# Kernel optimization log

Measured on AMD Instinct MI355X. Metric: run time of the kernel, lower is better.

## Reference

```python
import jax, jax.numpy as jnp
import numpy as np

B, N, DIM, H, HD, MLP = 32, 257, 1024, 16, 64, 4096
SCALE = HD ** -0.5


def _ln(x, w, b, eps=1e-5):
    m = x.mean(-1, keepdims=True)
    v = ((x - m) ** 2).mean(-1, keepdims=True)
    return (x - m) * jax.lax.rsqrt(v + eps) * w + b


def _quick_gelu(x):
    return x * jax.nn.sigmoid(1.702 * x)


def setup_inputs() -> dict:
    key = jax.random.key(0)
    ks = jax.random.split(key, 8)
    p = lambda k, s: jax.random.normal(k, s, jnp.float32) * 0.02
    return {
        'hidden_states': jax.random.normal(ks[0], (B, N, DIM), jnp.float32),
        'ln1_w': jnp.ones((DIM,), jnp.float32), 'ln1_b': jnp.zeros((DIM,), jnp.float32),
        'Wq': p(ks[1], (DIM, DIM)), 'bq': jnp.zeros((DIM,), jnp.float32),
        'Wk': p(ks[2], (DIM, DIM)), 'bk': jnp.zeros((DIM,), jnp.float32),
        'Wv': p(ks[3], (DIM, DIM)), 'bv': jnp.zeros((DIM,), jnp.float32),
        'Wo': p(ks[4], (DIM, DIM)), 'bo': jnp.zeros((DIM,), jnp.float32),
        'ln2_w': jnp.ones((DIM,), jnp.float32), 'ln2_b': jnp.zeros((DIM,), jnp.float32),
        'fc1_w': p(ks[5], (MLP, DIM)), 'fc1_b': jnp.zeros((MLP,), jnp.float32),
        'fc2_w': p(ks[6], (DIM, MLP)), 'fc2_b': jnp.zeros((DIM,), jnp.float32),
    }


def reference(hidden_states, ln1_w, ln1_b, Wq, bq, Wk, bk, Wv, bv, Wo, bo,
              ln2_w, ln2_b, fc1_w, fc1_b, fc2_w, fc2_b):
    x = _ln(hidden_states, ln1_w, ln1_b)            # [B,N,DIM]
    def heads(y):                                    # [B,N,DIM] -> [B,H,N,HD]
        return y.reshape(B, N, H, HD).transpose(0, 2, 1, 3)
    q = heads((x @ Wq.T + bq) * SCALE)
    k = heads(x @ Wk.T + bk)
    v = heads(x @ Wv.T + bv)
    attn_weights = jax.nn.softmax(jnp.einsum('bhnd,bhmd->bhnm', q, k), axis=-1)  # [B,H,N,N]
    ctx = jnp.einsum('bhnm,bhmd->bhnd', attn_weights, v)
    pre_proj = ctx.transpose(0, 2, 1, 3).reshape(B, N, DIM)
    attn_output = pre_proj @ Wo.T + bo
    h = hidden_states + attn_output
    residual = h
    h = _ln(h, ln2_w, ln2_b)
    h = _quick_gelu(h @ fc1_w.T + fc1_b) @ fc2_w.T + fc2_b
    hidden_out = residual + h
    # reuse_start='before_mlp': returns (pre_proj, cache_states=None, hidden, attn_weights, qkvs=None, reuse_map=None)
    return pre_proj, hidden_out, attn_weights
```

## Files before the change

kernel.cpp:

```cpp
#include <hip/hip_runtime.h>

typedef unsigned short u16;
typedef __bf16 bf16x8 __attribute__((ext_vector_type(8)));
typedef float f32x4 __attribute__((ext_vector_type(4)));
typedef unsigned short u16x8 __attribute__((ext_vector_type(8)));
typedef unsigned short u16x4 __attribute__((ext_vector_type(4)));

#define NBATCH 32
#define NTOK   257
#define DMODEL 1024
#define NHEAD  16
#define HDIM   64
#define DMLP   4096
#define MTOK   (NBATCH*NTOK)
#define MPAD   8320

__device__ __forceinline__ u16 f2bf(float f){
    unsigned int u = __float_as_uint(f);
    u = u + 0x7fffu + ((u >> 16) & 1u);
    return (u16)(u >> 16);
}

__device__ __forceinline__ f32x4 mfma16(bf16x8 a, bf16x8 b, f32x4 c){
    return __builtin_amdgcn_mfma_f32_16x16x32_bf16(a, b, c, 0, 0, 0);
}

__device__ __forceinline__ void gload16(const void* g, void* l){
    __builtin_amdgcn_global_load_lds(
        (const __attribute__((address_space(1))) unsigned int*)g,
        (__attribute__((address_space(3))) unsigned int*)l, 16, 0, 0);
}

__device__ __forceinline__ float waveSum64(float v){
    #pragma unroll
    for (int d = 1; d < 64; d <<= 1) v += __shfl_xor(v, d);
    return v;
}

__device__ __forceinline__ void xcd_swz(int &bx, int &by){
    int gx = gridDim.x;
    int nwg = gx * gridDim.y;
    int bid = blockIdx.y * gx + blockIdx.x;
    int wg = (bid & 7) * (nwg >> 3) + (bid >> 3);
    bx = wg % gx; by = wg / gx;
}

__global__ __launch_bounds__(256) void cvt_all(
        const float* __restrict__ wq, const float* __restrict__ wk,
        const float* __restrict__ wv, const float* __restrict__ wo,
        const float* __restrict__ f1, const float* __restrict__ f2,
        u16* __restrict__ dst){
    int b = blockIdx.x;
    const float* s; int rb; float sc = 1.0f;
    if (b < 1024)      { s = wq; rb = 0;    sc = 0.125f; }
    else if (b < 2048) { s = wk; rb = 1024; }
    else if (b < 3072) { s = wv; rb = 2048; }
    else if (b < 4096) { s = wo; rb = 3072; }
    else if (b < 8192) { s = f1; rb = 4096; }
    else               { s = f2; rb = 8192; }
    size_t li = ((size_t)(b - rb)*256 + threadIdx.x)*4;
    float4 v = *(const float4*)(s + li);
    u16x4 o = { f2bf(v.x*sc), f2bf(v.y*sc), f2bf(v.z*sc), f2bf(v.w*sc) };
    *(u16x4*)(dst + (size_t)b*1024 + threadIdx.x*4) = o;
}

__global__ __launch_bounds__(256) void build_bqkv(
        const float* __restrict__ bq, const float* __restrict__ bk,
        const float* __restrict__ bv, float* __restrict__ o){
    int i = blockIdx.x*256 + threadIdx.x;
    float v = (i < 1024) ? bq[i]*0.125f : ((i < 2048) ? bk[i-1024] : bv[i-2048]);
    o[i] = v;
}

__global__ __launch_bounds__(256) void ln_kernel(const float* __restrict__ x,
                                                 const float* __restrict__ w,
                                                 const float* __restrict__ b,
                                                 u16* __restrict__ y){
    int row = blockIdx.x, tid = threadIdx.x;
    float4 v = ((const float4*)(x + (size_t)row*DMODEL))[tid];
    float s = v.x + v.y + v.z + v.w;
    s = waveSum64(s);
    __shared__ float red[8];
    int wv = tid >> 6;
    if ((tid & 63) == 0) red[wv] = s;
    __syncthreads();
    float mean = (red[0]+red[1]+red[2]+red[3]) * (1.0f/1024.0f);
    float dx = v.x-mean, dy = v.y-mean, dz = v.z-mean, dw = v.w-mean;
    float s2 = dx*dx + dy*dy + dz*dz + dw*dw;
    s2 = waveSum64(s2);
    if ((tid & 63) == 0) red[4+wv] = s2;
    __syncthreads();
    float var = (red[4]+red[5]+red[6]+red[7]) * (1.0f/1024.0f);
    float rs = rsqrtf(var + 1e-5f);
    float4 wl = ((const float4*)w)[tid];
    float4 bl = ((const float4*)b)[tid];
    u16x4 o = { f2bf(dx*rs*wl.x + bl.x), f2bf(dy*rs*wl.y + bl.y),
                f2bf(dz*rs*wl.z + bl.z), f2bf(dw*rs*wl.w + bl.w) };
    ((u16x4*)(y + (size_t)row*DMODEL))[tid] = o;
}

template<int EPI>
__global__ __launch_bounds__(256) void gemm_bt(
        const u16* __restrict__ A, const u16* __restrict__ Wt,
        const float* __restrict__ bias, u16* __restrict__ outb,
        int K, int Nn, int Mvalid){
    __shared__ __align__(16) u16 As[128*64];
    __shared__ __align__(16) u16 Bs[128*64];
    int tid = threadIdx.x, lane = tid & 63, w = tid >> 6;
    int wr = w >> 1, wc = w & 1;
    int bx, by; xcd_swz(bx, by);
    int m0 = by*128, n0 = bx*128;
    int lrow = lane & 15, lk = lane >> 4;
    const f32x4 fz = {0.f,0.f,0.f,0.f};
    f32x4 acc[4][4];
    #pragma unroll
    for (int i = 0; i < 4; i++)
        #pragma unroll
        for (int j = 0; j < 4; j++) acc[i][j] = fz;

    const size_t Ks = (size_t)K;
    int so = w*1024 + lane*16;
    for (int kt = 0; kt < K; kt += 64){
        #pragma unroll
        for (int i = 0; i < 4; i++){
            int o = i*4096 + so;
            int row = o >> 7;
            int gsl = ((o >> 4) & 7) ^ (row & 7);
            gload16(A  + (size_t)(m0+row)*Ks + kt + gsl*8, &As[i*2048 + w*512]);
            gload16(Wt + (size_t)(n0+row)*Ks + kt + gsl*8, &Bs[i*2048 + w*512]);
        }
        __syncthreads();
        #pragma unroll
        for (int kk = 0; kk < 2; kk++){
            bf16x8 af[4], bfr[4];
            #pragma unroll
            for (int mi = 0; mi < 4; mi++){
                int row = wr*64 + mi*16 + lrow;
                int sl = (kk*4 + lk) ^ (row & 7);
                af[mi] = *(const bf16x8*)&As[row*64 + sl*8];
            }
            #pragma unroll
            for (int ni = 0; ni < 4; ni++){
                int row = wc*64 + ni*16 + lrow;
                int sl = (kk*4 + lk) ^ (row & 7);
                bfr[ni] = *(const bf16x8*)&Bs[row*64 + sl*8];
            }
            #pragma unroll
            for (int mi = 0; mi < 4; mi++)
                #pragma unroll
                for (int ni = 0; ni < 4; ni++)
                    acc[mi][ni] = mfma16(af[mi], bfr[ni], acc[mi][ni]);
        }
        __syncthreads();
    }
    #pragma unroll
    for (int mi = 0; mi < 4; mi++){
        #pragma unroll
        for (int ni = 0; ni < 4; ni++){
            int col = n0 + wc*64 + ni*16 + lrow;
            float bi = bias[col];
            #pragma unroll
            for (int r = 0; r < 4; r++){
                int row = m0 + wr*64 + mi*16 + lk*4 + r;
                if (row < Mvalid){
                    float v = acc[mi][ni][r] + bi;
                    size_t idx = (size_t)row*Nn + col;
                    if (EPI == 0){
                        outb[idx] = f2bf(v);
                    } else {
                        float g = v / (1.f + __expf(-1.702f*v));
                        outb[idx] = f2bf(g);
                    }
                }
            }
        }
    }
}

__global__ __launch_bounds__(256) void gemm_n64(
        const u16* __restrict__ A, const u16* __restrict__ Wt,
        const float* __restrict__ bias, const float* __restrict__ addsrc,
        float* __restrict__ outf,
        int K, int Nn, int Mvalid){
    __shared__ __align__(16) u16 As[128*64];
    __shared__ __align__(16) u16 Bs[64*64];
    int tid = threadIdx.x, lane = tid & 63, w = tid >> 6;
    int wr = w >> 1, wc = w & 1;
    int bx, by; xcd_swz(bx, by);
    int m0 = by*128, n0 = bx*64;
    int lrow = lane & 15, lk = lane >> 4;
    const f32x4 fz = {0.f,0.f,0.f,0.f};
    f32x4 acc[4][2];
    #pragma unroll
    for (int i = 0; i < 4; i++){ acc[i][0] = fz; acc[i][1] = fz; }

    const size_t Ks = (size_t)K;
    int so = w*1024 + lane*16;
    for (int kt = 0; kt < K; kt += 64){
        #pragma unroll
        for (int i = 0; i < 4; i++){
            int o = i*4096 + so;
            int row = o >> 7;
            int gsl = ((o >> 4) & 7) ^ (row & 7);
            gload16(A + (size_t)(m0+row)*Ks + kt + gsl*8, &As[i*2048 + w*512]);
        }
        #pragma unroll
        for (int i = 0; i < 2; i++){
            int o = i*4096 + so;
            int row = o >> 7;
            int gsl = ((o >> 4) & 7) ^ (row & 7);
            gload16(Wt + (size_t)(n0+row)*Ks + kt + gsl*8, &Bs[i*2048 + w*512]);
        }
        __syncthreads();
        #pragma unroll
        for (int kk = 0; kk < 2; kk++){
            bf16x8 af[4], bfr[2];
            #pragma unroll
            for (int mi = 0; mi < 4; mi++){
                int row = wr*64 + mi*16 + lrow;
                int sl = (kk*4 + lk) ^ (row & 7);
                af[mi] = *(const bf16x8*)&As[row*64 + sl*8];
            }
            #pragma unroll
            for (int ni = 0; ni < 2; ni++){
                int row = wc*32 + ni*16 + lrow;
                int sl = (kk*4 + lk) ^ (row & 7);
                bfr[ni] = *(const bf16x8*)&Bs[row*64 + sl*8];
            }
            #pragma unroll
            for (int mi = 0; mi < 4; mi++)
                #pragma unroll
                for (int ni = 0; ni < 2; ni++)
                    acc[mi][ni] = mfma16(af[mi], bfr[ni], acc[mi][ni]);
        }
        __syncthreads();
    }
    #pragma unroll
    for (int mi = 0; mi < 4; mi++){
        #pragma unroll
        for (int ni = 0; ni < 2; ni++){
            int col = n0 + wc*32 + ni*16 + lrow;
            float bi = bias[col];
            #pragma unroll
            for (int r = 0; r < 4; r++){
                int row = m0 + wr*64 + mi*16 + lk*4 + r;
                if (row < Mvalid){
                    float v = acc[mi][ni][r] + bi;
                    size_t idx = (size_t)row*Nn + col;
                    outf[idx] = addsrc[idx] + v;
                }
            }
        }
    }
}

__global__ __launch_bounds__(256) void attn_kernel(
        const u16* __restrict__ qkv, float* __restrict__ preproj,
        u16* __restrict__ ctxb, float* __restrict__ attnw){
    __shared__ __align__(16) u16 shm[18432 + 64*296];
    u16* Klds = shm;
    u16* Plds = shm;
    u16* Vt   = shm + 18432;
    int tid = threadIdx.x, lane = tid & 63, w = tid >> 6;
    int bh = blockIdx.x, bq = bh >> 4, hh = bh & 15;
    int q0 = blockIdx.y*64;
    int lrow = lane & 15, lk = lane >> 4;

    size_t base3 = ((size_t)bq*NTOK)*3072 + hh*HDIM;
    for (int c = tid; c < 2176; c += 256){
        int row = c >> 3, slot = c & 7;
        u16x8 kv = {0,0,0,0,0,0,0,0}, vv = {0,0,0,0,0,0,0,0};
        if (row < NTOK){
            kv = *(const u16x8*)(qkv + base3 + 1024 + (size_t)row*3072 + slot*8);
            vv = *(const u16x8*)(qkv + base3 + 2048 + (size_t)row*3072 + slot*8);
        }
        *(u16x8*)&Klds[row*64 + (slot ^ (row & 7))*8] = kv;
        int vr = (row < 256) ? (row ^ (slot << 3)) : row;
        #pragma unroll
        for (int j = 0; j < 8; j++) Vt[(slot*8 + j)*296 + vr] = vv[j];
    }
    for (int i = tid; i < 1536; i += 256){
        int d = i/24, c2 = 272 + (i - d*24);
        Vt[d*296 + c2] = 0;
    }
    int tok = bq*NTOK + q0 + w*16 + lrow;
    const u16* qp = qkv + (size_t)tok*3072 + hh*HDIM;
    bf16x8 qf0 = *(const bf16x8*)(qp + lk*8);
    bf16x8 qf1 = *(const bf16x8*)(qp + 32 + lk*8);
    __syncthreads();

    f32x4 S[17];
    __builtin_amdgcn_s_setprio(1);
    #pragma unroll
    for (int j = 0; j < 17; j++){
        int kcol = j*16 + lrow;
        f32x4 a = {0.f,0.f,0.f,0.f};
        bf16x8 b0 = *(const bf16x8*)&Klds[kcol*64 + ((0 + lk) ^ (kcol & 7))*8];
        a = mfma16(qf0, b0, a);
        bf16x8 b1 = *(const bf16x8*)&Klds[kcol*64 + ((4 + lk) ^ (kcol & 7))*8];
        S[j] = mfma16(qf1, b1, a);
    }
    __builtin_amdgcn_s_setprio(0);
    #pragma unroll
    for (int r = 0; r < 4; r++){
        float mx = -1e30f;
        #pragma unroll
        for (int j = 0; j < 17; j++){
            bool valid = (j < 16) || (lrow == 0);
            mx = fmaxf(mx, valid ? S[j][r] : -1e30f);
        }
        #pragma unroll
        for (int d = 1; d < 16; d <<= 1) mx = fmaxf(mx, __shfl_xor(mx, d));
        float sum = 0.f;
        #pragma unroll
        for (int j = 0; j < 17; j++){
            bool valid = (j < 16) || (lrow == 0);
            float p = valid ? __expf(S[j][r] - mx) : 0.f;
            S[j][r] = p; sum += p;
        }
        #pragma unroll
        for (int d = 1; d < 16; d <<= 1) sum += __shfl_xor(sum, d);
        float inv = 1.f / sum;
        #pragma unroll
        for (int j = 0; j < 17; j++) S[j][r] *= inv;
    }
    __syncthreads();

    for (int idx = tid; idx < 1024; idx += 256){
        int prow = idx >> 4, kk = idx & 15;
        int koff = 16 + kk;
        int slot = ((koff >> 3) ^ (prow >> 2)) & 3;
        Plds[8*2048 + prow*32 + slot*8 + (koff & 7)] = 0;
    }
    #pragma unroll
    for (int r = 0; r < 4; r++){
        int rw = lk*4 + r;
        int qrow = q0 + w*16 + rw;
        bool rowok = qrow < NTOK;
        size_t obase = ((size_t)bh*NTOK + qrow)*NTOK;
        int prow = w*16 + rw;
        #pragma unroll
        for (int j = 0; j < 17; j++){
            int col = j*16 + lrow;
            float p = S[j][r];
            if (rowok && col < NTOK) attnw[obase + col] = p;
            int kstep = col >> 5, koff = col & 31;
            int slot = ((koff >> 3) ^ (prow >> 2)) & 3;
            Plds[kstep*2048 + prow*32 + slot*8 + (koff & 7)] = f2bf(p);
        }
    }
    __syncthreads();

    f32x4 C4[4];
    #pragma unroll
    for (int n = 0; n < 4; n++) C4[n] = (f32x4){0.f,0.f,0.f,0.f};
    __builtin_amdgcn_s_setprio(1);
    #pragma unroll
    for (int ks = 0; ks < 9; ks++){
        int prow = w*16 + lrow;
        int slotp = (lk ^ (lrow >> 2)) & 3;
        bf16x8 pf = *(const bf16x8*)&Plds[ks*2048 + prow*32 + slotp*8];
        #pragma unroll
        for (int n = 0; n < 4; n++){
            int d = n*16 + lrow;
            int xv = (d >> 3) & 7;
            int kbase = ks*32 + lk*8;
            int kl = (ks < 8) ? (kbase ^ (xv << 3)) : kbase;
            bf16x8 vf = *(const bf16x8*)&Vt[d*296 + kl];
            C4[n] = mfma16(pf, vf, C4[n]);
        }
    }
    __builtin_amdgcn_s_setprio(0);
    #pragma unroll
    for (int n = 0; n < 4; n++){
        #pragma unroll
        for (int r = 0; r < 4; r++){
            int qrow = q0 + w*16 + lk*4 + r;
            if (qrow < NTOK){
                int tok2 = bq*NTOK + qrow;
                int d = hh*HDIM + n*16 + lrow;
                float v = C4[n][r];
                preproj[(size_t)tok2*DMODEL + d] = v;
                ctxb[(size_t)tok2*DMODEL + d] = f2bf(v);
            }
        }
    }
}

extern "C" void kernel_launch(void* const* d_in, const int* in_sizes, int n_in,
                              void* d_out, int out_size, void* d_ws, size_t ws_size,
                              hipStream_t stream){
    const float* hidden = (const float*)d_in[0];
    const float* ln1w = (const float*)d_in[1];
    const float* ln1b = (const float*)d_in[2];
    const float* Wq   = (const float*)d_in[3];
    const float* bq   = (const float*)d_in[4];
    const float* Wk   = (const float*)d_in[5];
    const float* bk   = (const float*)d_in[6];
    const float* Wv   = (const float*)d_in[7];
    const float* bv   = (const float*)d_in[8];
    const float* Wo   = (const float*)d_in[9];
    const float* bo   = (const float*)d_in[10];
    const float* ln2w = (const float*)d_in[11];
    const float* ln2b = (const float*)d_in[12];
    const float* fc1w = (const float*)d_in[13];
    const float* fc1b = (const float*)d_in[14];
    const float* fc2w = (const float*)d_in[15];
    const float* fc2b = (const float*)d_in[16];

    float* out0 = (float*)d_out;
    float* out1 = out0 + (size_t)MTOK*DMODEL;
    float* out2 = out1 + (size_t)MTOK*DMODEL;

    char* ws = (char*)d_ws;
    u16* qkvb = (u16*)ws;
    u16* fc1o = (u16*)ws;
    size_t off = (size_t)MPAD*DMLP*2;
    u16* xln  = (u16*)(ws + off);
    u16* ctxb = xln;
    off += (size_t)MPAD*DMODEL*2;
    u16* wbase = (u16*)(ws + off);
    u16* wqkv = wbase;
    u16* wob  = wbase + 3*1048576;
    u16* wf1  = wbase + 4*1048576;
    u16* wf2  = wbase + 8*1048576;
    off += (size_t)12*1048576*2;
    float* bqkv = (float*)(ws + off);

    cvt_all<<<12288, 256, 0, stream>>>(Wq, Wk, Wv, Wo, fc1w, fc2w, wbase);
    build_bqkv<<<12, 256, 0, stream>>>(bq, bk, bv, bqkv);

    ln_kernel<<<MTOK, 256, 0, stream>>>(hidden, ln1w, ln1b, xln);

    gemm_bt<0><<<dim3(24,65), 256, 0, stream>>>(xln, wqkv, bqkv, qkvb, 1024, 3072, MTOK);

    attn_kernel<<<dim3(512,5), 256, 0, stream>>>(qkvb, out0, ctxb, out2);

    gemm_n64<<<dim3(16,65), 256, 0, stream>>>(ctxb, wob, bo, hidden, out1, 1024, 1024, MTOK);

    ln_kernel<<<MTOK, 256, 0, stream>>>(out1, ln2w, ln2b, xln);

    gemm_bt<2><<<dim3(32,65), 256, 0, stream>>>(xln, wf1, fc1b, fc1o, 1024, 4096, MTOK);

    gemm_n64<<<dim3(16,65), 256, 0, stream>>>(fc1o, wf2, fc2b, out1, out1, 4096, 1024, MTOK);
}
```

Baseline: 470.2 us.

## Replace 128x128 GEMM with 256x256 tile, 4-stage LDS pipelined kernel for QKV and FC1

Swaps the single-buffered 128x128 bf16 GEMM used for the QKV and FC1 projections for a 512-thread, 256x256-tile kernel. The new kernel keeps a 4-slot LDS ring with K-steps of 32, issues loads three stages ahead, waits with explicit vmcnt, and raises wave priority around the MFMA block. It also uses a new XCD-aware block remap and pads M to 8448 so it divides into 256-row tiles. The goal is more reuse per loaded tile and overlap of global loads with compute, at the cost of far more LDS and registers, lower occupancy and more wasted padded rows.

```diff
diff --git a/kernel.cpp b/kernel.cpp
--- a/kernel.cpp
+++ b/kernel.cpp
@@ -13,7 +13,7 @@
 #define HDIM   64
 #define DMLP   4096
 #define MTOK   (NBATCH*NTOK)
-#define MPAD   8320
+#define MPAD   8448
 
 __device__ __forceinline__ u16 f2bf(float f){
     unsigned int u = __float_as_uint(f);
@@ -100,73 +100,107 @@
 }
 
 template<int EPI>
-__global__ __launch_bounds__(256) void gemm_bt(
+__global__ __launch_bounds__(512, 2) void gemm256(
         const u16* __restrict__ A, const u16* __restrict__ Wt,
-        const float* __restrict__ bias, u16* __restrict__ outb,
+        const float* __restrict__ bias, const float* __restrict__ addsrc,
+        float* __restrict__ outf, u16* __restrict__ outb,
         int K, int Nn, int Mvalid){
-    __shared__ __align__(16) u16 As[128*64];
-    __shared__ __align__(16) u16 Bs[128*64];
+    __shared__ __align__(16) u16 LA[4][8192];
+    __shared__ __align__(16) u16 LB[4][8192];
     int tid = threadIdx.x, lane = tid & 63, w = tid >> 6;
-    int wr = w >> 1, wc = w & 1;
-    int bx, by; xcd_swz(bx, by);
-    int m0 = by*128, n0 = bx*128;
+    int wr = w >> 2, wc = w & 3;
     int lrow = lane & 15, lk = lane >> 4;
-    const f32x4 fz = {0.f,0.f,0.f,0.f};
-    f32x4 acc[4][4];
-    #pragma unroll
-    for (int i = 0; i < 4; i++)
-        #pragma unroll
-        for (int j = 0; j < 4; j++) acc[i][j] = fz;
+    int gx = gridDim.x, nwg = gx * gridDim.y;
+    int bid = blockIdx.y * gx + blockIdx.x;
+    int qq = nwg >> 3, r8 = nwg & 7, xcd = bid & 7, pos = bid >> 3;
+    int wg = (xcd < r8 ? xcd*(qq+1) : r8*(qq+1) + (xcd-r8)*qq) + pos;
+    int bx = wg % gx, by = wg / gx;
+    int m0 = by*256, n0 = bx*256;
 
     const size_t Ks = (size_t)K;
-    int so = w*1024 + lane*16;
-    for (int kt = 0; kt < K; kt += 64){
-        #pragma unroll
-        for (int i = 0; i < 4; i++){
-            int o = i*4096 + so;
-            int row = o >> 7;
-            int gsl = ((o >> 4) & 7) ^ (row & 7);
-            gload16(A  + (size_t)(m0+row)*Ks + kt + gsl*8, &As[i*2048 + w*512]);
-            gload16(Wt + (size_t)(n0+row)*Ks + kt + gsl*8, &Bs[i*2048 + w*512]);
-        }
-        __syncthreads();
-        #pragma unroll
-        for (int kk = 0; kk < 2; kk++){
-            bf16x8 af[4], bfr[4];
-            #pragma unroll
-            for (int mi = 0; mi < 4; mi++){
-                int row = wr*64 + mi*16 + lrow;
-                int sl = (kk*4 + lk) ^ (row & 7);
-                af[mi] = *(const bf16x8*)&As[row*64 + sl*8];
-            }
-            #pragma unroll
-            for (int ni = 0; ni < 4; ni++){
-                int row = wc*64 + ni*16 + lrow;
-                int sl = (kk*4 + lk) ^ (row & 7);
-                bfr[ni] = *(const bf16x8*)&Bs[row*64 + sl*8];
-            }
-            #pragma unroll
-            for (int mi = 0; mi < 4; mi++)
-                #pragma unroll
-                for (int ni = 0; ni < 4; ni++)
-                    acc[mi][ni] = mfma16(af[mi], bfr[ni], acc[mi][ni]);
-        }
-        __syncthreads();
-    }
-    #pragma unroll
-    for (int mi = 0; mi < 4; mi++){
+    int o = (w << 10) + (lane << 4);
+    int lr0 = o >> 6;
+    int ga = ((((o >> 4) & 3) ^ ((lr0 ^ (lr0 >> 2)) & 3)) << 3);
+    int da = w << 9;
+    const u16* pA0 = A  + (size_t)(m0 + lr0)*Ks + ga;
+    const u16* pA1 = A  + (size_t)(m0 + 128 + lr0)*Ks + ga;
+    const u16* pB0 = Wt + (size_t)(n0 + lr0)*Ks + ga;
+    const u16* pB1 = Wt + (size_t)(n0 + 128 + lr0)*Ks + ga;
+    int aoff[8], boff[4];
+    #pragma unroll
+    for (int mi = 0; mi < 8; mi++){
+        int row = wr*128 + mi*16 + lrow;
+        aoff[mi] = row*32 + ((lk ^ ((row ^ (row >> 2)) & 3)) << 3);
+    }
+    #pragma unroll
+    for (int ni = 0; ni < 4; ni++){
+        int row = wc*64 + ni*16 + lrow;
+        boff[ni] = row*32 + ((lk ^ ((row ^ (row >> 2)) & 3)) << 3);
+    }
+    f32x4 acc[8][4];
+    #pragma unroll
+    for (int mi = 0; mi < 8; mi++)
+        #pragma unroll
+        for (int ni = 0; ni < 4; ni++) acc[mi][ni] = (f32x4){0.f,0.f,0.f,0.f};
+
+#define STAGE(T_) { \
+    int slot_ = (T_) & 3; int kt_ = (T_) << 5; \
+    gload16(pA0 + kt_, &LA[slot_][da]); \
+    gload16(pA1 + kt_, &LA[slot_][4096 + da]); \
+    gload16(pB0 + kt_, &LB[slot_][da]); \
+    gload16(pB1 + kt_, &LB[slot_][4096 + da]); }
+
+#define COMPUTE(SLOT_) { \
+    const u16* Ab_ = &LA[SLOT_][0]; const u16* Bb_ = &LB[SLOT_][0]; \
+    bf16x8 af[8]; bf16x8 bv[4]; \
+    _Pragma("unroll") \
+    for (int mi = 0; mi < 8; mi++) af[mi] = *(const bf16x8*)(Ab_ + aoff[mi]); \
+    _Pragma("unroll") \
+    for (int ni = 0; ni < 4; ni++) bv[ni] = *(const bf16x8*)(Bb_ + boff[ni]); \
+    __builtin_amdgcn_s_setprio(1); \
+    _Pragma("unroll") \
+    for (int mi = 0; mi < 8; mi++) \
+        _Pragma("unroll") \
+        for (int ni = 0; ni < 4; ni++) \
+            acc[mi][ni] = mfma16(af[mi], bv[ni], acc[mi][ni]); \
+    __builtin_amdgcn_s_setprio(0); }
+
+    int ns = K >> 5;
+    STAGE(0); STAGE(1); STAGE(2);
+    for (int s = 0; s < ns - 2; s++){
+        asm volatile("s_waitcnt vmcnt(8)" ::: "memory");
+        __builtin_amdgcn_s_barrier();
+        __builtin_amdgcn_sched_barrier(0);
+        if (s + 3 < ns) STAGE(s + 3);
+        COMPUTE(s & 3);
+    }
+    asm volatile("s_waitcnt vmcnt(4)" ::: "memory");
+    __builtin_amdgcn_s_barrier();
+    __builtin_amdgcn_sched_barrier(0);
+    COMPUTE((ns - 2) & 3);
+    asm volatile("s_waitcnt vmcnt(0)" ::: "memory");
+    __builtin_amdgcn_s_barrier();
+    __builtin_amdgcn_sched_barrier(0);
+    COMPUTE((ns - 1) & 3);
+#undef STAGE
+#undef COMPUTE
+
+    #pragma unroll
+    for (int mi = 0; mi < 8; mi++){
         #pragma unroll
         for (int ni = 0; ni < 4; ni++){
             int col = n0 + wc*64 + ni*16 + lrow;
             float bi = bias[col];
             #pragma unroll
-            for (int r = 0; r < 4; r++){
-                int row = m0 + wr*64 + mi*16 + lk*4 + r;
+            for (int rr = 0; rr < 4; rr++){
+                int row = m0 + wr*128 + mi*16 + lk*4 + rr;
                 if (row < Mvalid){
-                    float v = acc[mi][ni][r] + bi;
+                    float v = acc[mi][ni][rr] + bi;
                     size_t idx = (size_t)row*Nn + col;
                     if (EPI == 0){
                         outb[idx] = f2bf(v);
+                    } else if (EPI == 1){
+                        outf[idx] = addsrc[idx] + v;
                     } else {
                         float g = v / (1.f + __expf(-1.702f*v));
                         outb[idx] = f2bf(g);
@@ -432,7 +466,8 @@
 
     ln_kernel<<<MTOK, 256, 0, stream>>>(hidden, ln1w, ln1b, xln);
 
-    gemm_bt<0><<<dim3(24,65), 256, 0, stream>>>(xln, wqkv, bqkv, qkvb, 1024, 3072, MTOK);
+    gemm256<0><<<dim3(12,33), 512, 0, stream>>>(xln, wqkv, bqkv, nullptr,
+                                                nullptr, qkvb, 1024, 3072, MTOK);
 
     attn_kernel<<<dim3(512,5), 256, 0, stream>>>(qkvb, out0, ctxb, out2);
 
@@ -440,7 +475,8 @@
 
     ln_kernel<<<MTOK, 256, 0, stream>>>(out1, ln2w, ln2b, xln);
 
-    gemm_bt<2><<<dim3(32,65), 256, 0, stream>>>(xln, wf1, fc1b, fc1o, 1024, 4096, MTOK);
+    gemm256<2><<<dim3(16,33), 512, 0, stream>>>(xln, wf1, fc1b, nullptr,
+                                                nullptr, fc1o, 1024, 4096, MTOK);
 
     gemm_n64<<<dim3(16,65), 256, 0, stream>>>(fc1o, wf2, fc2b, out1, out1, 4096, 1024, MTOK);
 }
```

After: 541.2 us. +15.1%, slower.
